# Performance work log

Measured on AMD Instinct MI355X. Metric: run time of the kernel, lower is better.

The kernel has to match this reference:

```python
import jax, jax.numpy as jnp
import numpy as np

H = 3584          # hidden_size
NH = 28           # num query heads
NKV = 4           # num kv heads
HD = H // NH      # head_dim = 128
I = 18944         # intermediate_size
EPS = 1e-6
THETA = 1000000.0


def setup_inputs() -> dict:
    key = jax.random.key(0)
    ks = jax.random.split(key, 16)
    B, S = 1, 2048
    s = 0.02
    inp = {
        "hidden_states": jax.random.normal(ks[0], (B, S, H), jnp.float32),
        "position_ids": jnp.broadcast_to(jnp.arange(S, dtype=jnp.int32)[None, :], (B, S)),
        "q_w": jax.random.normal(ks[1], (NH * HD, H), jnp.float32) * s,
        "q_b": jax.random.normal(ks[2], (NH * HD,), jnp.float32) * s,
        "k_w": jax.random.normal(ks[3], (NKV * HD, H), jnp.float32) * s,
        "k_b": jax.random.normal(ks[4], (NKV * HD,), jnp.float32) * s,
        "v_w": jax.random.normal(ks[5], (NKV * HD, H), jnp.float32) * s,
        "v_b": jax.random.normal(ks[6], (NKV * HD,), jnp.float32) * s,
        "o_w": jax.random.normal(ks[7], (H, NH * HD), jnp.float32) * s,
        "gate_w": jax.random.normal(ks[8], (I, H), jnp.float32) * s,
        "up_w": jax.random.normal(ks[9], (I, H), jnp.float32) * s,
        "down_w": jax.random.normal(ks[10], (H, I), jnp.float32) * s,
        "ln1_w": jnp.ones((H,), jnp.float32),
        "ln2_w": jnp.ones((H,), jnp.float32),
    }
    return inp


def _rms_norm(x, w):
    var = jnp.mean(jnp.square(x), axis=-1, keepdims=True)
    return x * jax.lax.rsqrt(var + EPS) * w


def _rope_cos_sin(position_ids):
    # inv_freq: [HD/2]
    inv_freq = 1.0 / (THETA ** (jnp.arange(0, HD, 2, dtype=jnp.float32) / HD))
    ang = position_ids.astype(jnp.float32)[..., None] * inv_freq  # [B,S,HD/2]
    emb = jnp.concatenate([ang, ang], axis=-1)                     # [B,S,HD]
    return jnp.cos(emb)[:, None], jnp.sin(emb)[:, None]            # [B,1,S,HD]


def _rotate_half(x):
    x1, x2 = x[..., : HD // 2], x[..., HD // 2 :]
    return jnp.concatenate([-x2, x1], axis=-1)


def _forward(hidden_states, position_ids, q_w, q_b, k_w, k_b, v_w, v_b,
             o_w, gate_w, up_w, down_w, ln1_w, ln2_w):
    B, S, _ = hidden_states.shape
    residual = hidden_states
    x = _rms_norm(hidden_states, ln1_w)

    q = jnp.einsum("bsh,dh->bsd", x, q_w) + q_b   # [B,S,NH*HD]
    k = jnp.einsum("bsh,dh->bsd", x, k_w) + k_b   # [B,S,NKV*HD]
    v = jnp.einsum("bsh,dh->bsd", x, v_w) + v_b

    q = q.reshape(B, S, NH, HD).transpose(0, 2, 1, 3)    # [B,NH,S,HD]
    k = k.reshape(B, S, NKV, HD).transpose(0, 2, 1, 3)   # [B,NKV,S,HD]
    v = v.reshape(B, S, NKV, HD).transpose(0, 2, 1, 3)

    cos, sin = _rope_cos_sin(position_ids)
    q = q * cos + _rotate_half(q) * sin
    k = k * cos + _rotate_half(k) * sin

    # GQA: group query heads per kv head (NH = NKV * G)
    G = NH // NKV
    qg = q.reshape(B, NKV, G, S, HD)
    scores = jnp.einsum("bhgsd,bhtd->bhgst", qg, k) / jnp.sqrt(jnp.float32(HD))
    probs = jax.nn.softmax(scores, axis=-1)               # no causal mask in source
    attn = jnp.einsum("bhgst,bhtd->bhgsd", probs, v)      # [B,NKV,G,S,HD]
    attn = attn.reshape(B, NH, S, HD).transpose(0, 2, 1, 3).reshape(B, S, H)

    attn_out = jnp.einsum("bsd,hd->bsh", attn, o_w)
    hidden = residual + attn_out

    residual = hidden
    x = _rms_norm(hidden, ln2_w)
    gate = jax.nn.silu(jnp.einsum("bsh,ih->bsi", x, gate_w))
    up = jnp.einsum("bsh,ih->bsi", x, up_w)
    mlp = jnp.einsum("bsi,hi->bsh", gate * up, down_w)
    return residual + mlp


def reference(hidden_states, position_ids, q_w, q_b, k_w, k_b, v_w, v_b,
              o_w, gate_w, up_w, down_w, ln1_w, ln2_w):
    return _forward(hidden_states, position_ids, q_w, q_b, k_w, k_b, v_w, v_b,
                    o_w, gate_w, up_w, down_w, ln1_w, ln2_w)
```

## Files before the change

kernel.cpp:

```cpp
#include <hip/hip_runtime.h>
#include <hip/hip_bf16.h>
#include <stdint.h>

#define S_LEN 2048
#define HDIM  3584
#define NHEAD 28
#define NKVH  4
#define HDHD  128
#define IDIM  18944

typedef __attribute__((ext_vector_type(8))) short short8;
typedef __attribute__((ext_vector_type(4))) float floatx4;
typedef __attribute__((ext_vector_type(4))) unsigned int uint4v;

__device__ __forceinline__ unsigned short f2bf(float f) {
  union { float f; unsigned int u; } v; v.f = f;
  unsigned int r = v.u + 0x7fffu + ((v.u >> 16) & 1u);
  return (unsigned short)(r >> 16);
}
__device__ __forceinline__ float bf2f(unsigned short h) {
  union { unsigned int u; float f; } v; v.u = ((unsigned int)h) << 16;
  return v.f;
}
__device__ __forceinline__ unsigned int pk2(float a, float b) {
  __hip_bfloat162 h = __float22bfloat162_rn(make_float2(a, b));
  union { __hip_bfloat162 h; unsigned int u; } c; c.h = h; return c.u;
}

__device__ __forceinline__ void gload_lds16(const void* g, void* l) {
  __builtin_amdgcn_global_load_lds(
      (const __attribute__((address_space(1))) void*)g,
      (__attribute__((address_space(3))) void*)l, 16, 0, 0);
}

__device__ __forceinline__ int xcd_remap(int id, int total) {
  return (id & 7) * (total >> 3) + (id >> 3);
}

__device__ __forceinline__ void store_out(int MODE, void* outp, const void* aux,
                                          size_t oidx, float v) {
  if (MODE == 0) {
    ((float*)outp)[oidx] = v;
  } else if (MODE == 1) {
    ((unsigned short*)outp)[oidx] = f2bf(v);
  } else if (MODE == 2) {
    ((float*)outp)[oidx] = v + ((const float*)aux)[oidx];
  } else {
    float gt = bf2f(((const unsigned short*)aux)[oidx]);
    float sg = gt / (1.f + __expf(-gt));
    ((unsigned short*)outp)[oidx] = f2bf(sg * v);
  }
}

template<int MODE, bool BIAS>
__global__ __launch_bounds__(256)
void gemm_bf(const unsigned short* __restrict__ A, int lda,
             const unsigned short* __restrict__ W,
             const float* __restrict__ bias,
             void* __restrict__ outp, int ldo, int col0,
             const void* __restrict__ aux, int K)
{
  const int g  = xcd_remap(blockIdx.x, gridDim.x);
  const int mb = g & 15;
  const int nb = g >> 4;
  const int t = threadIdx.x;
  const int w = t >> 6, l = t & 63, lg = l >> 4, lc = l & 15;
  const int wr = w >> 1, wc = w & 1;

  __shared__ __align__(16) unsigned short As[128 * 64];
  __shared__ __align__(16) unsigned short Ws[128 * 64];

  floatx4 acc[4][4] = {};

  const char* Ablk = (const char*)(A + (size_t)mb * 128 * lda);
  const char* Wblk = (const char*)(W + (size_t)nb * 128 * K);

  const int s_row = t >> 3;
  const int s_scb = (((t & 7) ^ ((t >> 3) & 7)) << 4);
  const int r_sw  = (lc & 7) << 4;

  const size_t abytes = (size_t)lda * 2;
  const size_t wbytes = (size_t)K * 2;
  const int nk = K >> 6;
  for (int kt = 0; kt < nk; ++kt) {
    #pragma unroll
    for (int i = 0; i < 4; ++i)
      gload_lds16(Ablk + (size_t)(i * 32 + s_row) * abytes + (size_t)kt * 128 + s_scb,
                  (char*)As + i * 4096 + t * 16);
    #pragma unroll
    for (int i = 0; i < 4; ++i)
      gload_lds16(Wblk + (size_t)(i * 32 + s_row) * wbytes + (size_t)kt * 128 + s_scb,
                  (char*)Ws + i * 4096 + t * 16);
    __syncthreads();
    #pragma unroll
    for (int kk = 0; kk < 2; ++kk) {
      short8 afr[4], bfr[4];
      #pragma unroll
      for (int m = 0; m < 4; ++m)
        afr[m] = *(const short8*)((const char*)As + (wr*64 + m*16 + lc) * 128
                                 + ((kk*64 + lg*16) ^ r_sw));
      #pragma unroll
      for (int n = 0; n < 4; ++n)
        bfr[n] = *(const short8*)((const char*)Ws + (wc*64 + n*16 + lc) * 128
                                  + ((kk*64 + lg*16) ^ r_sw));
      #pragma unroll
      for (int m = 0; m < 4; ++m)
        #pragma unroll
        for (int n = 0; n < 4; ++n)
          acc[m][n] = __builtin_amdgcn_mfma_f32_16x16x32_bf16(afr[m], bfr[n], acc[m][n], 0, 0, 0);
    }
    __syncthreads();
  }

  float bv[4] = {0.f, 0.f, 0.f, 0.f};
  if (BIAS) {
    #pragma unroll
    for (int n = 0; n < 4; ++n) bv[n] = bias[nb*128 + wc*64 + n*16 + lc];
  }
  #pragma unroll
  for (int m = 0; m < 4; ++m) {
    #pragma unroll
    for (int n = 0; n < 4; ++n) {
      const int colg = col0 + nb*128 + wc*64 + n*16 + lc;
      #pragma unroll
      for (int j = 0; j < 4; ++j) {
        const int rowg = mb*128 + wr*64 + m*16 + lg*4 + j;
        store_out(MODE, outp, aux, (size_t)rowg * ldo + colg, acc[m][n][j] + bv[n]);
      }
    }
  }
}

template<int MODE, bool BIAS>
__global__ __launch_bounds__(256, 2)
void gemm_w(const unsigned short* __restrict__ A, int lda,
            const unsigned short* __restrict__ W,
            const float* __restrict__ bias,
            void* __restrict__ outp, int ldo, int col0,
            const void* __restrict__ aux, int K)
{
  const int g  = xcd_remap(blockIdx.x, gridDim.x);
  const int mb = g & 7;
  const int nb = g >> 3;
  const int t  = threadIdx.x;
  const int w  = t >> 6, l = t & 63, lg = l >> 4, lc = l & 15;
  const int wr = w >> 1, wc = w & 1;

  __shared__ __align__(16) unsigned short As[256 * 64];
  __shared__ __align__(16) unsigned short Bs[128 * 64];

  floatx4 acc[8][4] = {};

  const char* Ablk = (const char*)(A + (size_t)mb * 256 * lda);
  const char* Wblk = (const char*)(W + (size_t)nb * 128 * K);

  const int s_row = t >> 3;
  const int s_scb = (((t & 7) ^ ((t >> 3) & 7)) << 4);
  const int r_sw  = (lc & 7) << 4;

  const size_t abytes = (size_t)lda * 2;
  const size_t wbytes = (size_t)K * 2;
  const int nk = K >> 6;

  for (int kt = 0; kt < nk; ++kt) {
    const char* asrc = Ablk + (size_t)kt * 128 + s_scb;
    #pragma unroll
    for (int i = 0; i < 8; ++i)
      gload_lds16(asrc + (size_t)(i * 32 + s_row) * abytes,
                  (char*)As + i * 4096 + t * 16);
    const char* wsrc = Wblk + (size_t)kt * 128 + s_scb;
    #pragma unroll
    for (int i = 0; i < 4; ++i)
      gload_lds16(wsrc + (size_t)(i * 32 + s_row) * wbytes,
                  (char*)Bs + i * 4096 + t * 16);
    __syncthreads();
    #pragma unroll
    for (int kk = 0; kk < 2; ++kk) {
      const int ko = (kk * 64 + lg * 16) ^ r_sw;
      short8 bfr[4];
      #pragma unroll
      for (int n = 0; n < 4; ++n)
        bfr[n] = *(const short8*)((const char*)Bs + (wc*64 + n*16 + lc) * 128 + ko);
      #pragma unroll
      for (int m = 0; m < 8; ++m) {
        short8 af = *(const short8*)((const char*)As + (wr*128 + m*16 + lc) * 128 + ko);
        #pragma unroll
        for (int n = 0; n < 4; ++n)
          acc[m][n] = __builtin_amdgcn_mfma_f32_16x16x32_bf16(af, bfr[n], acc[m][n], 0, 0, 0);
      }
    }
    __syncthreads();
  }

  float bv[4] = {0.f, 0.f, 0.f, 0.f};
  if (BIAS) {
    #pragma unroll
    for (int n = 0; n < 4; ++n) bv[n] = bias[nb*128 + wc*64 + n*16 + lc];
  }
  #pragma unroll
  for (int m = 0; m < 8; ++m) {
    #pragma unroll
    for (int n = 0; n < 4; ++n) {
      const int colg = col0 + nb*128 + wc*64 + n*16 + lc;
      #pragma unroll
      for (int j = 0; j < 4; ++j) {
        const int rowg = mb*256 + wr*128 + m*16 + lg*4 + j;
        store_out(MODE, outp, aux, (size_t)rowg * ldo + colg, acc[m][n][j] + bv[n]);
      }
    }
  }
}

__global__ __launch_bounds__(256)
void cvt_bf16_kernel(const float* __restrict__ in, unsigned short* __restrict__ out, int n8)
{
  int i = blockIdx.x * 256 + threadIdx.x;
  const int stride = gridDim.x * 256;
  for (; i < n8; i += stride) {
    floatx4 a = *(const floatx4*)(in + (size_t)i * 8);
    floatx4 b = *(const floatx4*)(in + (size_t)i * 8 + 4);
    uint4v p;
    p[0] = pk2(a[0], a[1]); p[1] = pk2(a[2], a[3]);
    p[2] = pk2(b[0], b[1]); p[3] = pk2(b[2], b[3]);
    *(uint4v*)(out + (size_t)i * 8) = p;
  }
}

__global__ void pack_bias_kernel(const float* __restrict__ qb, const float* __restrict__ kb,
                                 const float* __restrict__ vb, float* __restrict__ o)
{
  int i = blockIdx.x * 256 + threadIdx.x;
  if (i < 3584) o[i] = qb[i];
  else if (i < 4096) o[i] = kb[i - 3584];
  else if (i < 4608) o[i] = vb[i - 4096];
}

__global__ __launch_bounds__(448)
void rmsnorm_kernel(const float* __restrict__ x, const float* __restrict__ wgt,
                    unsigned short* __restrict__ out)
{
  const int row = blockIdx.x, t = threadIdx.x;
  const float* xp = x + (size_t)row * HDIM + t * 8;
  floatx4 a = *(const floatx4*)xp;
  floatx4 b = *(const floatx4*)(xp + 4);
  float ss = a[0]*a[0]+a[1]*a[1]+a[2]*a[2]+a[3]*a[3]
           + b[0]*b[0]+b[1]*b[1]+b[2]*b[2]+b[3]*b[3];
  #pragma unroll
  for (int mk = 1; mk < 64; mk <<= 1) ss += __shfl_xor(ss, mk, 64);
  __shared__ float wsum[8];
  if ((t & 63) == 0) wsum[t >> 6] = ss;
  __syncthreads();
  float tot = 0.f;
  #pragma unroll
  for (int i = 0; i < 7; ++i) tot += wsum[i];
  const float sc = rsqrtf(tot * (1.f / 3584.f) + 1e-6f);
  const float* wp = wgt + t * 8;
  short8 o;
  #pragma unroll
  for (int e = 0; e < 4; ++e) o[e]   = (short)f2bf(a[e] * sc * wp[e]);
  #pragma unroll
  for (int e = 0; e < 4; ++e) o[4+e] = (short)f2bf(b[e] * sc * wp[4+e]);
  *(short8*)(out + (size_t)row * HDIM + t * 8) = o;
}

__global__ __launch_bounds__(448)
void add_rmsnorm_kernel(const float* __restrict__ x, const float* __restrict__ y,
                        const float* __restrict__ wgt,
                        float* __restrict__ h1, unsigned short* __restrict__ out)
{
  const int row = blockIdx.x, t = threadIdx.x;
  const size_t base = (size_t)row * HDIM + t * 8;
  floatx4 a = *(const floatx4*)(x + base);
  floatx4 b = *(const floatx4*)(x + base + 4);
  floatx4 c = *(const floatx4*)(y + base);
  floatx4 d = *(const floatx4*)(y + base + 4);
  a += c; b += d;
  *(floatx4*)(h1 + base)     = a;
  *(floatx4*)(h1 + base + 4) = b;
  float ss = a[0]*a[0]+a[1]*a[1]+a[2]*a[2]+a[3]*a[3]
           + b[0]*b[0]+b[1]*b[1]+b[2]*b[2]+b[3]*b[3];
  #pragma unroll
  for (int mk = 1; mk < 64; mk <<= 1) ss += __shfl_xor(ss, mk, 64);
  __shared__ float wsum[8];
  if ((t & 63) == 0) wsum[t >> 6] = ss;
  __syncthreads();
  float tot = 0.f;
  #pragma unroll
  for (int i = 0; i < 7; ++i) tot += wsum[i];
  const float sc = rsqrtf(tot * (1.f / 3584.f) + 1e-6f);
  const float* wp = wgt + t * 8;
  short8 o;
  #pragma unroll
  for (int e = 0; e < 4; ++e) o[e]   = (short)f2bf(a[e] * sc * wp[e]);
  #pragma unroll
  for (int e = 0; e < 4; ++e) o[4+e] = (short)f2bf(b[e] * sc * wp[4+e]);
  *(short8*)(out + (size_t)row * HDIM + t * 8) = o;
}

__global__ void rope_table_kernel(const int* __restrict__ pos, float* __restrict__ tab)
{
  int idx = blockIdx.x * 256 + threadIdx.x;
  int s = idx >> 6, d = idx & 63;
  float p = (float)pos[s];
  float inv = expf(-((float)(2 * d) * (1.f / 128.f)) * 13.815510557964274f);
  float ang = p * inv;
  tab[idx] = cosf(ang);
  tab[S_LEN * 64 + idx] = sinf(ang);
}

template<int NHX>
__global__ void rope_apply_kernel(const float* __restrict__ in, const float* __restrict__ tab,
                                  unsigned short* __restrict__ out, int col0)
{
  int idx = blockIdx.x * 256 + threadIdx.x;
  int d = idx & 63;
  int rem = idx >> 6;
  int hh = rem % NHX;
  int s  = rem / NHX;
  const float* ip = in + (size_t)s * 4608 + col0 + hh * HDHD;
  float x1 = ip[d], x2 = ip[64 + d];
  float c  = tab[s * 64 + d];
  float sn = tab[S_LEN * 64 + s * 64 + d];
  unsigned short* op = out + (size_t)s * (NHX * HDHD) + hh * HDHD;
  op[d]      = f2bf(x1 * c - x2 * sn);
  op[64 + d] = f2bf(x2 * c + x1 * sn);
}

__global__ void vtrans_kernel(const float* __restrict__ qkvf, unsigned short* __restrict__ vt)
{
  int idx = blockIdx.x * 256 + threadIdx.x;
  int s = idx & (S_LEN - 1);
  int c = idx >> 11;
  vt[idx] = f2bf(qkvf[(size_t)s * 4608 + 4096 + c]);
}

__global__ __launch_bounds__(512)
void attn_kernel(const unsigned short* __restrict__ Q,
                 const unsigned short* __restrict__ Kr,
                 const unsigned short* __restrict__ Vt,
                 unsigned short* __restrict__ O)
{
  const int g  = xcd_remap(blockIdx.x, gridDim.x);
  const int qb = g & 15;
  const int h  = g >> 4;
  const int kvh = h / 7;
  const int t = threadIdx.x, w = t >> 6, l = t & 63, lg = l >> 4, lc = l & 15;

  __shared__ __align__(16) unsigned short Ks[64 * 128];
  __shared__ __align__(16) unsigned short Vs[128 * 64];
  __shared__ __align__(16) unsigned short Ps[8][16 * 64];

  const int qrow = qb * 128 + w * 16 + lc;
  short8 qf[4];
  {
    const unsigned short* qp = Q + (size_t)qrow * HDIM + h * HDHD + lg * 8;
    #pragma unroll
    for (int kk = 0; kk < 4; ++kk) qf[kk] = *(const short8*)(qp + kk * 32);
  }

  float mrun[4], lrun[4];
  #pragma unroll
  for (int j = 0; j < 4; ++j) { mrun[j] = -1e30f; lrun[j] = 0.f; }
  floatx4 oacc[8] = {};

  const int k_row = t >> 4;
  const int k_scb = (((t & 15) ^ ((t >> 4) & 7)) << 4);
  const int v_row = t >> 3;
  const int v_scb = (((t & 7) ^ ((t >> 3) & 7)) << 4);
  const int r_sw  = (lc & 7) << 4;
  const float scale = 0.08838834764831843f;

  for (int kt = 0; kt < 32; ++kt) {
    #pragma unroll
    for (int i = 0; i < 2; ++i)
      gload_lds16((const char*)Kr + ((size_t)(kt*64 + i*32 + k_row) * 512 + kvh*128) * 2 + k_scb,
                  (char*)Ks + i * 8192 + t * 16);
    #pragma unroll
    for (int i = 0; i < 2; ++i)
      gload_lds16((const char*)Vt + ((size_t)(kvh*128 + i*64 + v_row) * S_LEN) * 2
                      + (size_t)kt * 128 + v_scb,
                  (char*)Vs + i * 8192 + t * 16);
    __syncthreads();

    floatx4 sacc[4] = {};
    #pragma unroll
    for (int kk = 0; kk < 4; ++kk) {
      #pragma unroll
      for (int n = 0; n < 4; ++n) {
        short8 kf = *(const short8*)((const char*)Ks + (n*16 + lc) * 256
                                     + ((kk*64 + lg*16) ^ r_sw));
        sacc[n] = __builtin_amdgcn_mfma_f32_16x16x32_bf16(qf[kk], kf, sacc[n], 0, 0, 0);
      }
    }

    float pv[4][4], mt[4];
    #pragma unroll
    for (int j = 0; j < 4; ++j) {
      float a0 = sacc[0][j]*scale, a1 = sacc[1][j]*scale;
      float a2 = sacc[2][j]*scale, a3 = sacc[3][j]*scale;
      pv[0][j]=a0; pv[1][j]=a1; pv[2][j]=a2; pv[3][j]=a3;
      mt[j] = fmaxf(fmaxf(a0, a1), fmaxf(a2, a3));
    }
    #pragma unroll
    for (int mk = 1; mk < 16; mk <<= 1)
      #pragma unroll
      for (int j = 0; j < 4; ++j)
        mt[j] = fmaxf(mt[j], __shfl_xor(mt[j], mk, 16));

    float corr[4], rs[4];
    #pragma unroll
    for (int j = 0; j < 4; ++j) {
      float mn = fmaxf(mrun[j], mt[j]);
      corr[j] = __expf(mrun[j] - mn);
      mrun[j] = mn;
      rs[j] = 0.f;
    }
    #pragma unroll
    for (int n = 0; n < 4; ++n)
      #pragma unroll
      for (int j = 0; j < 4; ++j) {
        float p = __expf(pv[n][j] - mrun[j]);
        pv[n][j] = p; rs[j] += p;
      }
    #pragma unroll
    for (int mk = 1; mk < 16; mk <<= 1)
      #pragma unroll
      for (int j = 0; j < 4; ++j)
        rs[j] += __shfl_xor(rs[j], mk, 16);
    #pragma unroll
    for (int j = 0; j < 4; ++j) lrun[j] = lrun[j] * corr[j] + rs[j];
    #pragma unroll
    for (int q = 0; q < 8; ++q) {
      oacc[q][0] *= corr[0]; oacc[q][1] *= corr[1];
      oacc[q][2] *= corr[2]; oacc[q][3] *= corr[3];
    }

    char* pw = (char*)Ps[w];
    #pragma unroll
    for (int n = 0; n < 4; ++n)
      #pragma unroll
      for (int j = 0; j < 4; ++j) {
        const int prow = lg*4 + j;
        *(unsigned short*)(pw + prow*128 + ((((n*16 + lc)*2)) ^ ((prow & 7) << 4)))
            = f2bf(pv[n][j]);
      }

    short8 pa[2];
    #pragma unroll
    for (int ks = 0; ks < 2; ++ks)
      pa[ks] = *(const short8*)(pw + lc*128 + ((ks*64 + lg*16) ^ r_sw));
    #pragma unroll
    for (int ks = 0; ks < 2; ++ks)
      #pragma unroll
      for (int q = 0; q < 8; ++q) {
        short8 vf = *(const short8*)((const char*)Vs + (q*16 + lc) * 128
                                     + ((ks*64 + lg*16) ^ r_sw));
        oacc[q] = __builtin_amdgcn_mfma_f32_16x16x32_bf16(pa[ks], vf, oacc[q], 0, 0, 0);
      }
    __syncthreads();
  }

  float invl[4];
  #pragma unroll
  for (int j = 0; j < 4; ++j) invl[j] = 1.f / lrun[j];
  #pragma unroll
  for (int q = 0; q < 8; ++q)
    #pragma unroll
    for (int j = 0; j < 4; ++j) {
      int rowg = qb*128 + w*16 + lg*4 + j;
      int colg = h*HDHD + q*16 + lc;
      O[(size_t)rowg * HDIM + colg] = f2bf(oacc[q][j] * invl[j]);
    }
}

__global__ void sentinel_kernel(float* out, int n) {
  int i = blockIdx.x * 256 + threadIdx.x;
  if (i < n) out[i] = 1.0e6f;
}

extern "C" void kernel_launch(void* const* d_in, const int* in_sizes, int n_in,
                              void* d_out, int out_size, void* d_ws, size_t ws_size,
                              hipStream_t stream)
{
  (void)in_sizes; (void)n_in;
  const float* hidden = (const float*)d_in[0];
  const int*   pos    = (const int*)d_in[1];
  const float* q_w    = (const float*)d_in[2];
  const float* q_b    = (const float*)d_in[3];
  const float* k_w    = (const float*)d_in[4];
  const float* k_b    = (const float*)d_in[5];
  const float* v_w    = (const float*)d_in[6];
  const float* v_b    = (const float*)d_in[7];
  const float* o_w    = (const float*)d_in[8];
  const float* gate_w = (const float*)d_in[9];
  const float* up_w   = (const float*)d_in[10];
  const float* down_w = (const float*)d_in[11];
  const float* ln1    = (const float*)d_in[12];
  const float* ln2    = (const float*)d_in[13];
  float* out = (float*)d_out;
  char* ws = (char*)d_ws;

  unsigned short* XN    = (unsigned short*)(ws + 0);
  float*          QKVF  = (float*)(ws + 14680064);
  unsigned short* QR    = (unsigned short*)(ws + 52428800);
  unsigned short* KR    = (unsigned short*)(ws + 67108864);
  unsigned short* VT    = (unsigned short*)(ws + 69206016);
  float*          ROPET = (float*)(ws + 71303168);
  float*          BQKV  = (float*)(ws + 72351744);
  unsigned short* CTX   = (unsigned short*)(ws + 77594624);
  float*          AO    = (float*)(ws + 92274688);
  unsigned short* GBUF  = (unsigned short*)(ws + 0);
  unsigned short* ACT   = (unsigned short*)(ws + 77594624);
  float*          H1    = (float*)(ws + 155189248);
  unsigned short* XN2   = (unsigned short*)(ws + 184549376);
  unsigned short* WB    = (unsigned short*)(ws + 199229440);
  const size_t NEED_BIG = 199229440 + 135790592;

  if (ws_size < NEED_BIG) {
    sentinel_kernel<<<(out_size + 255) / 256, 256, 0, stream>>>(out, out_size);
    return;
  }

  const int CVG = 2048;

  rope_table_kernel<<<(S_LEN * 64) / 256, 256, 0, stream>>>(pos, ROPET);
  rmsnorm_kernel<<<S_LEN, 448, 0, stream>>>(hidden, ln1, XN);

  pack_bias_kernel<<<18, 256, 0, stream>>>(q_b, k_b, v_b, BQKV);
  cvt_bf16_kernel<<<CVG, 256, 0, stream>>>(q_w, WB,               (3584 * 3584) / 8);
  cvt_bf16_kernel<<<CVG, 256, 0, stream>>>(k_w, WB + 3584 * 3584, (512 * 3584) / 8);
  cvt_bf16_kernel<<<CVG, 256, 0, stream>>>(v_w, WB + 4096 * 3584, (512 * 3584) / 8);

  gemm_w<0, true><<<288, 256, 0, stream>>>(XN, HDIM, WB, BQKV, QKVF, 4608, 0, nullptr, HDIM);

  rope_apply_kernel<28><<<(S_LEN * 28 * 64) / 256, 256, 0, stream>>>(QKVF, ROPET, QR, 0);
  rope_apply_kernel<4><<<(S_LEN * 4 * 64) / 256,  256, 0, stream>>>(QKVF, ROPET, KR, 3584);
  vtrans_kernel<<<(512 * S_LEN) / 256, 256, 0, stream>>>(QKVF, VT);

  cvt_bf16_kernel<<<CVG, 256, 0, stream>>>(o_w, WB, (3584 * 3584) / 8);

  attn_kernel<<<448, 512, 0, stream>>>(QR, KR, VT, CTX);

  gemm_w<0, false><<<224, 256, 0, stream>>>(CTX, HDIM, WB, nullptr, AO, HDIM, 0, nullptr, HDIM);
  add_rmsnorm_kernel<<<S_LEN, 448, 0, stream>>>(hidden, AO, ln2, H1, XN2);

  cvt_bf16_kernel<<<CVG, 256, 0, stream>>>(gate_w, WB, (IDIM * HDIM) / 8);
  gemm_w<1, false><<<1184, 256, 0, stream>>>(XN2, HDIM, WB, nullptr, GBUF, IDIM, 0, nullptr, HDIM);

  cvt_bf16_kernel<<<CVG, 256, 0, stream>>>(up_w, WB, (IDIM * HDIM) / 8);
  gemm_w<3, false><<<1184, 256, 0, stream>>>(XN2, HDIM, WB, nullptr, ACT, IDIM, 0, GBUF, HDIM);

  cvt_bf16_kernel<<<CVG, 256, 0, stream>>>(down_w, WB, (HDIM * IDIM) / 8);
  gemm_bf<2, false><<<448, 256, 0, stream>>>(ACT, IDIM, WB, nullptr, out, HDIM, 0, H1, IDIM);
}
```

Baseline: 1.652 ms.

## Add double-buffered K=32 GEMM kernel for gate and up projections

Adds a new GEMM kernel that double-buffers LDS tiles with a K-step of 32, issuing async global-to-LDS loads for the next tile while MFMAs run on the current one, using explicit waitcnt, barriers and setprio. It replaces the single-buffered gemm_w for the two large MLP gate and up projections. The aim is to hide global memory latency behind compute. In exchange the kernel runs more barrier iterations per K, uses a different LDS swizzle, and keeps the same LDS footprint.

```diff
diff --git a/kernel.cpp b/kernel.cpp
--- a/kernel.cpp
+++ b/kernel.cpp
@@ -190,6 +190,105 @@
       }
     }
     __syncthreads();
+  }
+
+  float bv[4] = {0.f, 0.f, 0.f, 0.f};
+  if (BIAS) {
+    #pragma unroll
+    for (int n = 0; n < 4; ++n) bv[n] = bias[nb*128 + wc*64 + n*16 + lc];
+  }
+  #pragma unroll
+  for (int m = 0; m < 8; ++m) {
+    #pragma unroll
+    for (int n = 0; n < 4; ++n) {
+      const int colg = col0 + nb*128 + wc*64 + n*16 + lc;
+      #pragma unroll
+      for (int j = 0; j < 4; ++j) {
+        const int rowg = mb*256 + wr*128 + m*16 + lg*4 + j;
+        store_out(MODE, outp, aux, (size_t)rowg * ldo + colg, acc[m][n][j] + bv[n]);
+      }
+    }
+  }
+}
+
+template<int MODE, bool BIAS>
+__global__ __launch_bounds__(256)
+void gemm_db32(const unsigned short* __restrict__ A, int lda,
+               const unsigned short* __restrict__ W,
+               const float* __restrict__ bias,
+               void* __restrict__ outp, int ldo, int col0,
+               const void* __restrict__ aux, int K)
+{
+  const int g  = xcd_remap(blockIdx.x, gridDim.x);
+  const int mb = g & 7;
+  const int nb = g >> 3;
+  const int t  = threadIdx.x;
+  const int w  = t >> 6, l = t & 63, lg = l >> 4, lc = l & 15;
+  const int wr = w >> 1, wc = w & 1;
+
+  __shared__ __align__(16) unsigned short As[2][256 * 32];
+  __shared__ __align__(16) unsigned short Bs[2][128 * 32];
+
+  floatx4 acc[8][4] = {};
+
+  const char* Ablk = (const char*)(A + (size_t)mb * 256 * lda);
+  const char* Wblk = (const char*)(W + (size_t)nb * 128 * K);
+
+  const int s_row = t >> 2;
+  const int s_scb = (((t & 3) ^ ((t >> 2) & 3)) << 4);
+  const int r_sw2 = (lc & 3) << 4;
+
+  const size_t abytes = (size_t)lda * 2;
+  const size_t wbytes = (size_t)K * 2;
+
+  auto stage = [&](int buf, int kt) {
+    const char* asrc = Ablk + (size_t)kt * 64 + s_scb;
+    #pragma unroll
+    for (int i = 0; i < 4; ++i)
+      gload_lds16(asrc + (size_t)(i * 64 + s_row) * abytes,
+                  (char*)As[buf] + i * 4096 + t * 16);
+    const char* wsrc = Wblk + (size_t)kt * 64 + s_scb;
+    #pragma unroll
+    for (int i = 0; i < 2; ++i)
+      gload_lds16(wsrc + (size_t)(i * 64 + s_row) * wbytes,
+                  (char*)Bs[buf] + i * 4096 + t * 16);
+  };
+
+  const int nk = K >> 5;
+  stage(0, 0);
+
+  for (int kt = 0; kt < nk; ++kt) {
+    const int cur = kt & 1;
+    if (kt + 1 < nk) {
+      stage(cur ^ 1, kt + 1);
+      asm volatile("s_waitcnt vmcnt(6)" ::: "memory");
+    } else {
+      asm volatile("s_waitcnt vmcnt(0)" ::: "memory");
+    }
+    __builtin_amdgcn_sched_barrier(0);
+    __builtin_amdgcn_s_barrier();
+    __builtin_amdgcn_sched_barrier(0);
+
+    const char* ac = (const char*)As[cur];
+    const char* bc = (const char*)Bs[cur];
+    const int ko = (lg << 4) ^ r_sw2;
+    short8 bfr[4];
+    #pragma unroll
+    for (int n = 0; n < 4; ++n)
+      bfr[n] = *(const short8*)(bc + (wc*64 + n*16 + lc) * 64 + ko);
+    __builtin_amdgcn_s_setprio(1);
+    #pragma unroll
+    for (int m = 0; m < 8; ++m) {
+      short8 af = *(const short8*)(ac + (wr*128 + m*16 + lc) * 64 + ko);
+      #pragma unroll
+      for (int n = 0; n < 4; ++n)
+        acc[m][n] = __builtin_amdgcn_mfma_f32_16x16x32_bf16(af, bfr[n], acc[m][n], 0, 0, 0);
+    }
+    __builtin_amdgcn_s_setprio(0);
+    asm volatile("s_waitcnt lgkmcnt(0)" ::: "memory");
+    __builtin_amdgcn_sched_barrier(0);
+    __builtin_amdgcn_s_barrier();
+    __builtin_amdgcn_sched_barrier(0);
   }
 
   float bv[4] = {0.f, 0.f, 0.f, 0.f};
@@ -545,10 +644,10 @@
   add_rmsnorm_kernel<<<S_LEN, 448, 0, stream>>>(hidden, AO, ln2, H1, XN2);
 
   cvt_bf16_kernel<<<CVG, 256, 0, stream>>>(gate_w, WB, (IDIM * HDIM) / 8);
-  gemm_w<1, false><<<1184, 256, 0, stream>>>(XN2, HDIM, WB, nullptr, GBUF, IDIM, 0, nullptr, HDIM);
+  gemm_db32<1, false><<<1184, 256, 0, stream>>>(XN2, HDIM, WB, nullptr, GBUF, IDIM, 0, nullptr, HDIM);
 
   cvt_bf16_kernel<<<CVG, 256, 0, stream>>>(up_w, WB, (IDIM * HDIM) / 8);
-  gemm_w<3, false><<<1184, 256, 0, stream>>>(XN2, HDIM, WB, nullptr, ACT, IDIM, 0, GBUF, HDIM);
+  gemm_db32<3, false><<<1184, 256, 0, stream>>>(XN2, HDIM, WB, nullptr, ACT, IDIM, 0, GBUF, HDIM);
 
   cvt_bf16_kernel<<<CVG, 256, 0, stream>>>(down_w, WB, (HDIM * IDIM) / 8);
   gemm_bf<2, false><<<448, 256, 0, stream>>>(ACT, IDIM, WB, nullptr, out, HDIM, 0, H1, IDIM);
```

Result: slower. 2.211 ms (+33.9%).

## Add 256x256-tile 8-wave GEMM with split-phase pipelining for gate projection

Applied to the files above, without the earlier changes.

Adds a new GEMM kernel with 512 threads that computes 256x256 output tiles, split into four 128x128 quadrants. Each quadrant's A and B halves load into double-buffered LDS separately, with staggered waitcnt/barrier phases so MFMA work on one quadrant overlaps the loads for the next k-step. The gate projection switches to this kernel with half as many blocks. The larger tile should cut global-memory traffic per FLOP, at the cost of more LDS and registers per block and lower occupancy.

```diff
diff --git a/kernel.cpp b/kernel.cpp
--- a/kernel.cpp
+++ b/kernel.cpp
@@ -209,6 +209,162 @@
       }
     }
   }
+}
+
+template<int MODE>
+__global__ __launch_bounds__(512)
+void gemm_8p(const unsigned short* __restrict__ A, int lda,
+             const unsigned short* __restrict__ W,
+             void* __restrict__ outp, int ldo,
+             const void* __restrict__ aux, int K)
+{
+  const int g  = xcd_remap(blockIdx.x, gridDim.x);
+  const int mb = g & 7;
+  const int nb = g >> 3;
+  const int t  = threadIdx.x;
+  const int w  = t >> 6, l = t & 63, lg = l >> 4, lc = l & 15;
+  const int wr = w >> 2;
+  const int wc = w & 3;
+
+  __shared__ __align__(16) unsigned short As[2][2][128 * 64];
+  __shared__ __align__(16) unsigned short Bs[2][2][128 * 64];
+
+  floatx4 acc[2][2][4][2] = {};
+
+  const char* Ablk = (const char*)(A + (size_t)mb * 256 * lda);
+  const char* Wblk = (const char*)(W + (size_t)nb * 256 * K);
+
+  const int s_row = t >> 3;
+  const int s_scb = (((t & 7) ^ ((t >> 3) & 7)) << 4);
+  const int r_sw  = (lc & 7) << 4;
+
+  const size_t abytes = (size_t)lda * 2;
+  const size_t wbytes = (size_t)K * 2;
+
+  auto stageh = [&](int buf, int kt, int op, int h) {
+    if (op == 0) {
+      const char* src = Ablk + (size_t)(h * 128) * abytes + (size_t)kt * 128 + s_scb;
+      char* dst = (char*)As[buf][h] + t * 16;
+      gload_lds16(src + (size_t)s_row * abytes, dst);
+      gload_lds16(src + (size_t)(64 + s_row) * abytes, dst + 8192);
+    } else {
+      const char* src = Wblk + (size_t)(h * 128) * wbytes + (size_t)kt * 128 + s_scb;
+      char* dst = (char*)Bs[buf][h] + t * 16;
+      gload_lds16(src + (size_t)s_row * wbytes, dst);
+      gload_lds16(src + (size_t)(64 + s_row) * wbytes, dst + 8192);
+    }
+  };
+
+  const int nk = K >> 6;
+  stageh(0, 0, 0, 0); stageh(0, 0, 1, 0); stageh(0, 0, 1, 1); stageh(0, 0, 0, 1);
+
+  short8 afr[4][2];
+  short8 b0[2][2];
+  short8 b1[2][2];
+
+  for (int j = 0; j < nk; ++j) {
+    const int buf = j & 1;
+    const bool more = (j + 1 < nk);
+    const char* a0 = (const char*)As[buf][0];
+    const char* a1 = (const char*)As[buf][1];
+    const char* bb0 = (const char*)Bs[buf][0];
+    const char* bb1 = (const char*)Bs[buf][1];
+
+    if (more) { stageh(buf ^ 1, j + 1, 0, 0);
+                asm volatile("s_waitcnt vmcnt(6)" ::: "memory"); }
+    else      { asm volatile("s_waitcnt vmcnt(4)" ::: "memory"); }
+    __builtin_amdgcn_sched_barrier(0);
+    __builtin_amdgcn_s_barrier();
+    __builtin_amdgcn_sched_barrier(0);
+    #pragma unroll
+    for (int m = 0; m < 4; ++m)
+      #pragma unroll
+      for (int kk = 0; kk < 2; ++kk)
+        afr[m][kk] = *(const short8*)(a0 + (wr*64 + m*16 + lc) * 128 + ((kk*64 + lg*16) ^ r_sw));
+    #pragma unroll
+    for (int n = 0; n < 2; ++n)
+      #pragma unroll
+      for (int kk = 0; kk < 2; ++kk)
+        b0[n][kk] = *(const short8*)(bb0 + (wc*32 + n*16 + lc) * 128 + ((kk*64 + lg*16) ^ r_sw));
+    __builtin_amdgcn_s_setprio(1);
+    #pragma unroll
+    for (int m = 0; m < 4; ++m)
+      #pragma unroll
+      for (int n = 0; n < 2; ++n)
+        #pragma unroll
+        for (int kk = 0; kk < 2; ++kk)
+          acc[0][0][m][n] = __builtin_amdgcn_mfma_f32_16x16x32_bf16(afr[m][kk], b0[n][kk], acc[0][0][m][n], 0, 0, 0);
+    __builtin_amdgcn_s_setprio(0);
+
+    if (more) { stageh(buf ^ 1, j + 1, 1, 0);
+                asm volatile("s_waitcnt vmcnt(6)" ::: "memory"); }
+    else      { asm volatile("s_waitcnt vmcnt(2)" ::: "memory"); }
+    __builtin_amdgcn_sched_barrier(0);
+    __builtin_amdgcn_s_barrier();
+    __builtin_amdgcn_sched_barrier(0);
+    #pragma unroll
+    for (int n = 0; n < 2; ++n)
+      #pragma unroll
+      for (int kk = 0; kk < 2; ++kk)
+        b1[n][kk] = *(const short8*)(bb1 + (wc*32 + n*16 + lc) * 128 + ((kk*64 + lg*16) ^ r_sw));
+    __builtin_amdgcn_s_setprio(1);
+    #pragma unroll
+    for (int m = 0; m < 4; ++m)
+      #pragma unroll
+      for (int n = 0; n < 2; ++n)
+        #pragma unroll
+        for (int kk = 0; kk < 2; ++kk)
+          acc[0][1][m][n] = __builtin_amdgcn_mfma_f32_16x16x32_bf16(afr[m][kk], b1[n][kk], acc[0][1][m][n], 0, 0, 0);
+    __builtin_amdgcn_s_setprio(0);
+
+    if (more) { stageh(buf ^ 1, j + 1, 1, 1);
+                asm volatile("s_waitcnt vmcnt(6)" ::: "memory"); }
+    else      { asm volatile("s_waitcnt vmcnt(0)" ::: "memory"); }
+    __builtin_amdgcn_sched_barrier(0);
+    __builtin_amdgcn_s_barrier();
+    __builtin_amdgcn_sched_barrier(0);
+    #pragma unroll
+    for (int m = 0; m < 4; ++m)
+      #pragma unroll
+      for (int kk = 0; kk < 2; ++kk)
+        afr[m][kk] = *(const short8*)(a1 + (wr*64 + m*16 + lc) * 128 + ((kk*64 + lg*16) ^ r_sw));
+    __builtin_amdgcn_s_setprio(1);
+    #pragma unroll
+    for (int m = 0; m < 4; ++m)
+      #pragma unroll
+      for (int n = 0; n < 2; ++n)
+        #pragma unroll
+        for (int kk = 0; kk < 2; ++kk)
+          acc[1][1][m][n] = __builtin_amdgcn_mfma_f32_16x16x32_bf16(afr[m][kk], b1[n][kk], acc[1][1][m][n], 0, 0, 0);
+    __builtin_amdgcn_s_setprio(0);
+
+    if (more) stageh(buf ^ 1, j + 1, 0, 1);
+    __builtin_amdgcn_s_setprio(1);
+    #pragma unroll
+    for (int m = 0; m < 4; ++m)
+      #pragma unroll
+      for (int n = 0; n < 2; ++n)
+        #pragma unroll
+        for (int kk = 0; kk < 2; ++kk)
+          acc[1][0][m][n] = __builtin_amdgcn_mfma_f32_16x16x32_bf16(afr[m][kk], b0[n][kk], acc[1][0][m][n], 0, 0, 0);
+    __builtin_amdgcn_s_setprio(0);
+  }
+
+  #pragma unroll
+  for (int qm = 0; qm < 2; ++qm)
+    #pragma unroll
+    for (int qn = 0; qn < 2; ++qn)
+      #pragma unroll
+      for (int m = 0; m < 4; ++m)
+        #pragma unroll
+        for (int n = 0; n < 2; ++n) {
+          const int colg = nb*256 + qn*128 + wc*32 + n*16 + lc;
+          #pragma unroll
+          for (int jj = 0; jj < 4; ++jj) {
+            const int rowg = mb*256 + qm*128 + wr*64 + m*16 + lg*4 + jj;
+            store_out(MODE, outp, aux, (size_t)rowg * ldo + colg, acc[qm][qn][m][n][jj]);
+          }
+        }
 }
 
 __global__ __launch_bounds__(256)
@@ -545,7 +701,7 @@
   add_rmsnorm_kernel<<<S_LEN, 448, 0, stream>>>(hidden, AO, ln2, H1, XN2);
 
   cvt_bf16_kernel<<<CVG, 256, 0, stream>>>(gate_w, WB, (IDIM * HDIM) / 8);
-  gemm_w<1, false><<<1184, 256, 0, stream>>>(XN2, HDIM, WB, nullptr, GBUF, IDIM, 0, nullptr, HDIM);
+  gemm_8p<1><<<592, 512, 0, stream>>>(XN2, HDIM, WB, GBUF, IDIM, nullptr, HDIM);
 
   cvt_bf16_kernel<<<CVG, 256, 0, stream>>>(up_w, WB, (IDIM * HDIM) / 8);
   gemm_w<3, false><<<1184, 256, 0, stream>>>(XN2, HDIM, WB, nullptr, ACT, IDIM, 0, GBUF, HDIM);
```

New measurement: 1.683 ms. About the same (+1.9%).
